# Performance work log

Measured on AMD Instinct MI355X. Metric: run time of the kernel, lower is better.

The kernel has to match this reference:

```python
import jax, jax.numpy as jnp
import numpy as np

B, T, M, P = 256, 256, 512, 512


def setup_inputs() -> dict:
    key = jax.random.key(0)
    ks = jax.random.split(key, 10)
    sc = lambda fan: 1.0 / np.sqrt(fan)
    return {
        "H": jax.random.normal(ks[0], (B, T, M), jnp.float32),
        "d0": jax.random.normal(ks[1], (1, B, P), jnp.float32),
        "s0": jax.random.normal(ks[2], (1, B, P), jnp.float32),
        # TemporalAttention params (torch Linear convention: y = x @ W.T)
        "W_d": jax.random.uniform(ks[3], (M, 2 * P), jnp.float32, -sc(2 * P), sc(2 * P)),
        "U_d": jax.random.uniform(ks[4], (M, M), jnp.float32, -sc(M), sc(M)),
        "v_d": jax.random.uniform(ks[5], (1, M), jnp.float32, -sc(M), sc(M)),
        # LSTM params (torch nn.LSTM convention, gate order i,f,g,o)
        "W_ih": jax.random.uniform(ks[6], (4 * P, M), jnp.float32, -sc(P), sc(P)),
        "W_hh": jax.random.uniform(ks[7], (4 * P, P), jnp.float32, -sc(P), sc(P)),
        "b_ih": jax.random.uniform(ks[8], (4 * P,), jnp.float32, -sc(P), sc(P)),
        "b_hh": jax.random.uniform(ks[9], (4 * P,), jnp.float32, -sc(P), sc(P)),
    }


def reference(H, d0, s0, W_d, U_d, v_d, W_ih, W_hh, b_ih, b_hh):
    T_steps = H.shape[1]
    # U_d(H) is time-invariant across decode steps: precompute once. [B,T,m]
    UH = jnp.einsum("btm,nm->btn", H, U_d)
    v = v_d[0]  # [m]

    def step(carry, _):
        d, s = carry  # [B,p] hidden, [B,p] cell
        q = jnp.concatenate([d, s], axis=-1)            # [B,2p]
        wq = q @ W_d.T                                   # [B,m]
        e = jnp.tanh(wq[:, None, :] + UH) @ v            # [B,T]
        beta = jax.nn.softmax(e, axis=1)                 # softmax over time
        c_t = jnp.einsum("bt,btm->bm", beta, H)          # [B,m]
        gates = c_t @ W_ih.T + b_ih + d @ W_hh.T + b_hh  # [B,4p]
        i, f, g, o = jnp.split(gates, 4, axis=-1)
        s_new = jax.nn.sigmoid(f) * s + jax.nn.sigmoid(i) * jnp.tanh(g)
        d_new = jax.nn.sigmoid(o) * jnp.tanh(s_new)
        return (d_new, s_new), (beta, c_t)

    (d, s), (betas, cts) = jax.lax.scan(step, (d0[0], s0[0]), None, length=T_steps)
    attn = jnp.transpose(betas, (1, 0, 2))               # [B,T,T]
    out = jnp.concatenate([d[:, None, :], cts[-1][:, None, :]], axis=2)  # [B,1,p+m]
    return out, attn
```

## Files before the change

kernel.cpp:

```cpp
#include <hip/hip_runtime.h>
#include <hip/hip_fp16.h>

typedef _Float16 h4 __attribute__((ext_vector_type(4)));
typedef _Float16 h8 __attribute__((ext_vector_type(8)));
typedef float    f4 __attribute__((ext_vector_type(4)));

#define SC2LOG2E 2.8853900817779268f

__device__ __forceinline__ float v_exp2(float x) { float r; asm("v_exp_f32 %0, %1" : "=v"(r) : "v"(x)); return r; }
__device__ __forceinline__ float v_rcp (float x) { float r; asm("v_rcp_f32 %0, %1" : "=v"(r) : "v"(x)); return r; }
__device__ __forceinline__ float fast_tanh(float x) {
    float e = __expf(2.0f * x);
    return 1.0f - 2.0f * v_rcp(e + 1.0f);
}
__device__ __forceinline__ float fast_sigmoid(float x) {
    return v_rcp(1.0f + __expf(-x));
}

__global__ void convert_f16(const float* __restrict__ s, _Float16* __restrict__ d, int n) {
    int i = (blockIdx.x * 256 + threadIdx.x) * 4;
    if (i < n) {
        float4 v = *(const float4*)(s + i);
        h4 o = {(_Float16)v.x, (_Float16)v.y, (_Float16)v.z, (_Float16)v.w};
        *(h4*)(d + i) = o;
    }
}

__global__ void build_wg(const float* __restrict__ Wih, const float* __restrict__ Whh,
                         _Float16* __restrict__ Wg) {
    int idx = (blockIdx.x * 256 + threadIdx.x) * 4;
    int np = idx >> 10, k = idx & 1023;
    int p = np >> 2, g = np & 3, row = g * 512 + p;
    const float* src = (k < 512) ? Wih + (size_t)row * 512 + k
                                 : Whh + (size_t)row * 512 + (k - 512);
    float4 v = *(const float4*)src;
    h4 o = {(_Float16)v.x, (_Float16)v.y, (_Float16)v.z, (_Float16)v.w};
    *(h4*)(Wg + idx) = o;
}

__global__ void build_bsum(const float* __restrict__ bih, const float* __restrict__ bhh,
                           float* __restrict__ bsum) {
    int np = blockIdx.x * 256 + threadIdx.x;
    int p = np >> 2, g = np & 3, row = g * 512 + p;
    bsum[np] = bih[row] + bhh[row];
}

__global__ void init_state(const float* __restrict__ d0, const float* __restrict__ s0,
                           float* __restrict__ sbuf,
                           _Float16* __restrict__ qA, _Float16* __restrict__ ds) {
    int i = blockIdx.x * 256 + threadIdx.x;
    float dv = d0[i], sv = s0[i];
    sbuf[i] = sv;
    int b = i >> 9, j = i & 511;
    qA[(size_t)b * 1024 + 512 + j] = (_Float16)dv;
    ds[(size_t)b * 1024 + j]       = (_Float16)dv;
    ds[(size_t)b * 1024 + 512 + j] = (_Float16)sv;
}

__global__ __launch_bounds__(128) void uh_mfma(const float* __restrict__ H,
                                               const float* __restrict__ Ud,
                                               _Float16* __restrict__ UH2) {
    int tid = threadIdx.x;
    int lane = tid & 63, w = tid >> 6;
    int ln = lane & 15, quad = lane >> 4;
    int m0 = blockIdx.x * 64, n0 = blockIdx.y * 32;
    f4 z = {0.f, 0.f, 0.f, 0.f};
    f4 acc[4] = {z, z, z, z};
    const float* brow = Ud + (size_t)(n0 + w * 16 + ln) * 512 + quad * 8;
    const float* arow = H  + (size_t)(m0 + ln) * 512 + quad * 8;
#pragma unroll 2
    for (int k = 0; k < 16; k++) {
        float4 bx = *(const float4*)(brow + k * 32);
        float4 by = *(const float4*)(brow + k * 32 + 4);
        h8 b = {(_Float16)bx.x, (_Float16)bx.y, (_Float16)bx.z, (_Float16)bx.w,
                (_Float16)by.x, (_Float16)by.y, (_Float16)by.z, (_Float16)by.w};
#pragma unroll
        for (int mt = 0; mt < 4; mt++) {
            const float* ap = arow + (size_t)mt * 16 * 512 + k * 32;
            float4 ax = *(const float4*)ap;
            float4 ay = *(const float4*)(ap + 4);
            h8 a = {(_Float16)ax.x, (_Float16)ax.y, (_Float16)ax.z, (_Float16)ax.w,
                    (_Float16)ay.x, (_Float16)ay.y, (_Float16)ay.z, (_Float16)ay.w};
            acc[mt] = __builtin_amdgcn_mfma_f32_16x16x32_f16(a, b, acc[mt], 0, 0, 0);
        }
    }
#pragma unroll
    for (int mt = 0; mt < 4; mt++)
#pragma unroll
        for (int r = 0; r < 4; r++)
            UH2[(size_t)(m0 + mt * 16 + quad * 4 + r) * 512 + n0 + w * 16 + ln] =
                (_Float16)(acc[mt][r] * SC2LOG2E);
}

__global__ __launch_bounds__(256) void wq_gemm(const _Float16* __restrict__ ds,
                                               const _Float16* __restrict__ Wdh,
                                               float* __restrict__ wq2) {
    int tid = threadIdx.x;
    int lane = tid & 63, w = tid >> 6;
    int ln = lane & 15, quad = lane >> 4;
    int m0 = blockIdx.x * 64, n0 = blockIdx.y * 16;
    f4 acc = {0.f, 0.f, 0.f, 0.f};
    const h8* ap = (const h8*)(ds  + (size_t)(m0 + w * 16 + ln) * 1024) + quad;
    const h8* bp = (const h8*)(Wdh + (size_t)(n0 + ln) * 1024) + quad;
#pragma unroll 8
    for (int k = 0; k < 32; k++) {
        h8 a = ap[k * 4];
        h8 b = bp[k * 4];
        acc = __builtin_amdgcn_mfma_f32_16x16x32_f16(a, b, acc, 0, 0, 0);
    }
#pragma unroll
    for (int r = 0; r < 4; r++)
        wq2[(size_t)(m0 + w * 16 + quad * 4 + r) * 512 + n0 + ln] = acc[r] * SC2LOG2E;
}

__global__ __launch_bounds__(512) void gates_gemm(const _Float16* __restrict__ qcur,
                                                  const _Float16* __restrict__ Wg,
                                                  const float* __restrict__ bsum,
                                                  float* __restrict__ sbuf,
                                                  _Float16* __restrict__ qnext,
                                                  _Float16* __restrict__ ds,
                                                  float* __restrict__ out,
                                                  int t) {
    __shared__ float gt[64][36];
    int tid = threadIdx.x;
    int lane = tid & 63, w = tid >> 6;
    int ln = lane & 15, quad = lane >> 4;
    int mt = w & 3, nt = w >> 2;
    int m0 = blockIdx.x * 64, n0 = blockIdx.y * 32;
    f4 acc = {0.f, 0.f, 0.f, 0.f};
    const h8* ap = (const h8*)(qcur + (size_t)(m0 + mt * 16 + ln) * 1024) + quad;
    const h8* bp = (const h8*)(Wg   + (size_t)(n0 + nt * 16 + ln) * 1024) + quad;
#pragma unroll 8
    for (int k = 0; k < 32; k++) {
        h8 a = ap[k * 4];
        h8 b = bp[k * 4];
        acc = __builtin_amdgcn_mfma_f32_16x16x32_f16(a, b, acc, 0, 0, 0);
    }
    float bs = bsum[n0 + nt * 16 + ln];
#pragma unroll
    for (int r = 0; r < 4; r++)
        gt[mt * 16 + quad * 4 + r][nt * 16 + ln] = acc[r] + bs;
    __syncthreads();

    int p0 = blockIdx.y * 8;
    int ml = tid >> 3, pl = tid & 7;
    float4 g4 = *(const float4*)&gt[ml][pl * 4];
    int b = m0 + ml, p = p0 + pl;
    float ig = fast_sigmoid(g4.x);
    float fg = fast_sigmoid(g4.y);
    float gg = fast_tanh(g4.z);
    float og = fast_sigmoid(g4.w);
    float sold = sbuf[(size_t)b * 512 + p];
    float snew = fmaf(fg, sold, ig * gg);
    float dnew = og * fast_tanh(snew);
    sbuf[(size_t)b * 512 + p] = snew;
    qnext[(size_t)b * 1024 + 512 + p] = (_Float16)dnew;
    ds[(size_t)b * 1024 + p]          = (_Float16)dnew;
    ds[(size_t)b * 1024 + 512 + p]    = (_Float16)snew;
    if (t == 255) out[(size_t)b * 1024 + p] = dnew;
}

__global__ __launch_bounds__(1024) void attn_kernel(const _Float16* __restrict__ UH2,
                                                    const _Float16* __restrict__ Hh,
                                                    const float* __restrict__ Hf,
                                                    const float* __restrict__ wq2,
                                                    const float* __restrict__ vd,
                                                    _Float16* __restrict__ qcur,
                                                    float* __restrict__ attn_out,
                                                    float* __restrict__ out,
                                                    int t) {
    __shared__ float es[256];
    __shared__ float red[4];
    __shared__ float red2[4];
    __shared__ float part[8][512];

    int b = blockIdx.x;
    int tid = threadIdx.x;
    int wv = tid >> 6, lane = tid & 63;

    const float4* wqp = (const float4*)(wq2 + (size_t)b * 512 + lane * 8);
    float4 w0 = wqp[0], w1 = wqp[1];
    const float4* vp = (const float4*)(vd + lane * 8);
    float4 vv0 = vp[0], vv1 = vp[1];
    float wr[8] = {w0.x, w0.y, w0.z, w0.w, w1.x, w1.y, w1.z, w1.w};
    float vr[8] = {vv0.x, vv0.y, vv0.z, vv0.w, vv1.x, vv1.y, vv1.z, vv1.w};

    const h8* up = (const h8*)(UH2 + (size_t)b * 256 * 512) + lane;
#pragma unroll 2
    for (int i = 0; i < 16; i++) {
        int tp = wv * 16 + i;
        h8 u = up[(size_t)tp * 64];
        float acc = 0.0f;
#pragma unroll
        for (int j = 0; j < 8; j++) {
            float zz = wr[j] + (float)u[j];
            float r = v_rcp(1.0f + v_exp2(zz));
            acc = fmaf(vr[j], r, acc);
        }
#pragma unroll
        for (int o = 32; o; o >>= 1) acc += __shfl_xor(acc, o, 64);
        if (lane == 0) es[tp] = -2.0f * acc;
    }
    __syncthreads();

    float v = 0.0f, ex = 0.0f;
    if (tid < 256) {
        v = es[tid];
        float mx = v;
#pragma unroll
        for (int o = 32; o; o >>= 1) mx = fmaxf(mx, __shfl_xor(mx, o, 64));
        if (lane == 0) red[wv] = mx;
    }
    __syncthreads();
    float mall = fmaxf(fmaxf(red[0], red[1]), fmaxf(red[2], red[3]));
    if (tid < 256) {
        ex = __expf(v - mall);
        float s = ex;
#pragma unroll
        for (int o = 32; o; o >>= 1) s += __shfl_xor(s, o, 64);
        if (lane == 0) red2[wv] = s;
    }
    __syncthreads();
    float tot = red2[0] + red2[1] + red2[2] + red2[3];
    float beta = 0.0f;
    if (tid < 256) beta = ex * v_rcp(tot);
    __syncthreads();
    if (tid < 256) {
        es[tid] = beta;
        attn_out[(size_t)b * 65536 + (size_t)t * 256 + tid] = beta;
    }
    __syncthreads();

    int tc = tid >> 7, g = tid & 127;
    float a0 = 0, a1 = 0, a2 = 0, a3 = 0;
    if (Hh) {
        const h4* hp = (const h4*)(Hh + ((size_t)b * 256 + tc * 32) * 512) + g;
#pragma unroll 4
        for (int i = 0; i < 32; i++) {
            h4 hv = hp[(size_t)i * 128];
            float bt = es[tc * 32 + i];
            a0 = fmaf(bt, (float)hv[0], a0);
            a1 = fmaf(bt, (float)hv[1], a1);
            a2 = fmaf(bt, (float)hv[2], a2);
            a3 = fmaf(bt, (float)hv[3], a3);
        }
    } else {
        const float4* hp = (const float4*)(Hf + ((size_t)b * 256 + tc * 32) * 512) + g;
#pragma unroll 4
        for (int i = 0; i < 32; i++) {
            float4 hv = hp[(size_t)i * 128];
            float bt = es[tc * 32 + i];
            a0 = fmaf(bt, hv.x, a0);
            a1 = fmaf(bt, hv.y, a1);
            a2 = fmaf(bt, hv.z, a2);
            a3 = fmaf(bt, hv.w, a3);
        }
    }
    *(float4*)&part[tc][g * 4] = make_float4(a0, a1, a2, a3);
    __syncthreads();
    if (tid < 512) {
        int m = tid;
        float c = part[0][m] + part[1][m] + part[2][m] + part[3][m]
                + part[4][m] + part[5][m] + part[6][m] + part[7][m];
        qcur[(size_t)b * 1024 + m] = (_Float16)c;
        if (t == 255) out[(size_t)b * 1024 + 512 + m] = c;
    }
}

extern "C" void kernel_launch(void* const* d_in, const int* in_sizes, int n_in,
                              void* d_out, int out_size, void* d_ws, size_t ws_size,
                              hipStream_t stream) {
    const float* H   = (const float*)d_in[0];
    const float* d0  = (const float*)d_in[1];
    const float* s0  = (const float*)d_in[2];
    const float* Wd  = (const float*)d_in[3];
    const float* Ud  = (const float*)d_in[4];
    const float* vd  = (const float*)d_in[5];
    const float* Wih = (const float*)d_in[6];
    const float* Whh = (const float*)d_in[7];
    const float* bih = (const float*)d_in[8];
    const float* bhh = (const float*)d_in[9];

    float* out  = (float*)d_out;
    float* attn = out + 262144;

    char* ws = (char*)d_ws;
    size_t off = 0;
    _Float16* UH2  = (_Float16*)(ws + off); off += 67108864;
    _Float16* Wdh  = (_Float16*)(ws + off); off += 1048576;
    _Float16* Wg   = (_Float16*)(ws + off); off += 4194304;
    float*    bsum = (float*)   (ws + off); off += 8192;
    float*    wq2  = (float*)   (ws + off); off += 524288;
    _Float16* qA   = (_Float16*)(ws + off); off += 524288;
    _Float16* qB   = (_Float16*)(ws + off); off += 524288;
    _Float16* ds   = (_Float16*)(ws + off); off += 524288;
    float*    sbuf = (float*)   (ws + off); off += 524288;
    _Float16* Hh   = nullptr;
    if (ws_size >= off + 67108864) { Hh = (_Float16*)(ws + off); off += 67108864; }

    convert_f16<<<512, 256, 0, stream>>>(Wd, Wdh, 524288);
    build_wg<<<2048, 256, 0, stream>>>(Wih, Whh, Wg);
    build_bsum<<<8, 256, 0, stream>>>(bih, bhh, bsum);
    if (Hh) convert_f16<<<32768, 256, 0, stream>>>(H, Hh, 33554432);
    init_state<<<512, 256, 0, stream>>>(d0, s0, sbuf, qA, ds);
    uh_mfma<<<dim3(1024, 16), 128, 0, stream>>>(H, Ud, UH2);

    for (int t = 0; t < 256; t++) {
        _Float16* qcur = (t & 1) ? qB : qA;
        _Float16* qnxt = (t & 1) ? qA : qB;
        wq_gemm<<<dim3(4, 32), 256, 0, stream>>>(ds, Wdh, wq2);
        attn_kernel<<<256, 1024, 0, stream>>>(UH2, Hh, H, wq2, vd, qcur, attn, out, t);
        gates_gemm<<<dim3(4, 64), 512, 0, stream>>>(qcur, Wg, bsum, sbuf, qnxt, ds, out, t);
    }
}
```

Before: 14.34 ms.

## Fuse per-step decoder kernels into one persistent cooperative kernel with grid barriers

Replaces the 768 per-step kernel launches (wq GEMM, attention, gates GEMM) with a single persistent cooperative kernel of 256 blocks of 512 threads. The three phases are separated by a custom atomic grid barrier. This removes launch overhead and inter-kernel gaps on the sequential recurrence. In exchange the attention phase runs with half as many threads per block, and correctness depends on all blocks being co-resident and on the spin barrier; there is a non-cooperative fallback launch.

```diff
diff --git a/kernel.cpp b/kernel.cpp
--- a/kernel.cpp
+++ b/kernel.cpp
@@ -55,6 +55,11 @@
     qA[(size_t)b * 1024 + 512 + j] = (_Float16)dv;
     ds[(size_t)b * 1024 + j]       = (_Float16)dv;
     ds[(size_t)b * 1024 + 512 + j] = (_Float16)sv;
+}
+
+__global__ void zero_bar(unsigned* __restrict__ bar, int n) {
+    int i = blockIdx.x * 256 + threadIdx.x;
+    if (i < n) bar[i] = 0u;
 }
 
 __global__ __launch_bounds__(128) void uh_mfma(const float* __restrict__ H,
@@ -92,178 +97,211 @@
                 (_Float16)(acc[mt][r] * SC2LOG2E);
 }
 
-__global__ __launch_bounds__(256) void wq_gemm(const _Float16* __restrict__ ds,
-                                               const _Float16* __restrict__ Wdh,
-                                               float* __restrict__ wq2) {
-    int tid = threadIdx.x;
-    int lane = tid & 63, w = tid >> 6;
-    int ln = lane & 15, quad = lane >> 4;
-    int m0 = blockIdx.x * 64, n0 = blockIdx.y * 16;
-    f4 acc = {0.f, 0.f, 0.f, 0.f};
-    const h8* ap = (const h8*)(ds  + (size_t)(m0 + w * 16 + ln) * 1024) + quad;
-    const h8* bp = (const h8*)(Wdh + (size_t)(n0 + ln) * 1024) + quad;
+__device__ __forceinline__ void gbar(unsigned* __restrict__ arrive,
+                                     unsigned* __restrict__ gen,
+                                     unsigned ticket) {
+    __syncthreads();
+    if (blockIdx.x == 0) {
+        int tid = threadIdx.x;
+        if (tid >= 1 && tid < 256) {
+            while (__hip_atomic_load(arrive + (size_t)tid * 16, __ATOMIC_RELAXED,
+                                     __HIP_MEMORY_SCOPE_AGENT) < ticket)
+                __builtin_amdgcn_s_sleep(1);
+        }
+        __builtin_amdgcn_fence(__ATOMIC_ACQUIRE, "agent");
+        __syncthreads();
+        if (tid == 0)
+            __hip_atomic_store(gen, ticket, __ATOMIC_RELEASE, __HIP_MEMORY_SCOPE_AGENT);
+    } else {
+        if (threadIdx.x == 0) {
+            __hip_atomic_store(arrive + (size_t)blockIdx.x * 16, ticket,
+                               __ATOMIC_RELEASE, __HIP_MEMORY_SCOPE_AGENT);
+            while (__hip_atomic_load(gen, __ATOMIC_RELAXED,
+                                     __HIP_MEMORY_SCOPE_AGENT) < ticket)
+                __builtin_amdgcn_s_sleep(1);
+        }
+        __builtin_amdgcn_fence(__ATOMIC_ACQUIRE, "agent");
+        __syncthreads();
+    }
+}
+
+struct LoopArgs {
+    const _Float16* UH2;
+    const _Float16* Hh;
+    const float*    Hf;
+    const _Float16* Wdh;
+    const _Float16* Wg;
+    const float*    bsum;
+    const float*    vd;
+    float*          wq2;
+    _Float16*       qA;
+    _Float16*       qB;
+    _Float16*       ds;
+    float*          sbuf;
+    float*          out;
+    float*          attn;
+    unsigned*       bar;
+};
+
+__global__ __launch_bounds__(512) void decoder_loop(LoopArgs A) {
+    const int bid = blockIdx.x;
+    const int tid = threadIdx.x;
+    const int lane = tid & 63, wv = tid >> 6;
+    const int ln = lane & 15, quad = lane >> 4;
+
+    __shared__ __align__(16) union {
+        struct { float es[256]; float red[4]; float red2[4]; float part[4][512]; } at;
+        float gt[64][36];
+    } sm;
+
+    unsigned* arrive = A.bar;
+    unsigned* gen    = A.bar + 4096;
+    unsigned  bt     = 0;
+
+    const int a_m0 = (bid >> 5) * 64, a_n0 = (bid & 31) * 16;
+    const float4* vp = (const float4*)(A.vd + lane * 8);
+    float4 vv0 = vp[0], vv1 = vp[1];
+    float vr[8] = {vv0.x, vv0.y, vv0.z, vv0.w, vv1.x, vv1.y, vv1.z, vv1.w};
+    const h8* up = (const h8*)(A.UH2 + (size_t)bid * 131072) + lane;
+    const int c_mt = wv & 3, c_nt = wv >> 2;
+    const int c_m0 = (bid & 3) * 64, c_by = bid >> 2;
+    const int c_n0 = c_by * 32, c_p0 = c_by * 8;
+    const float c_bs = A.bsum[c_n0 + c_nt * 16 + ln];
+    const int c_ml = tid >> 3, c_pl = tid & 7;
+
+#pragma unroll 1
+    for (int t = 0; t < 256; ++t) {
+        _Float16* qcur = (t & 1) ? A.qB : A.qA;
+        _Float16* qnxt = (t & 1) ? A.qA : A.qB;
+
+        if (bid < 128 && tid < 256) {
+            f4 acc = {0.f, 0.f, 0.f, 0.f};
+            const h8* ap = (const h8*)(A.ds  + (size_t)(a_m0 + wv * 16 + ln) * 1024) + quad;
+            const h8* bp = (const h8*)(A.Wdh + (size_t)(a_n0 + ln) * 1024) + quad;
 #pragma unroll 8
-    for (int k = 0; k < 32; k++) {
-        h8 a = ap[k * 4];
-        h8 b = bp[k * 4];
-        acc = __builtin_amdgcn_mfma_f32_16x16x32_f16(a, b, acc, 0, 0, 0);
-    }
-#pragma unroll
-    for (int r = 0; r < 4; r++)
-        wq2[(size_t)(m0 + w * 16 + quad * 4 + r) * 512 + n0 + ln] = acc[r] * SC2LOG2E;
-}
-
-__global__ __launch_bounds__(512) void gates_gemm(const _Float16* __restrict__ qcur,
-                                                  const _Float16* __restrict__ Wg,
-                                                  const float* __restrict__ bsum,
-                                                  float* __restrict__ sbuf,
-                                                  _Float16* __restrict__ qnext,
-                                                  _Float16* __restrict__ ds,
-                                                  float* __restrict__ out,
-                                                  int t) {
-    __shared__ float gt[64][36];
-    int tid = threadIdx.x;
-    int lane = tid & 63, w = tid >> 6;
-    int ln = lane & 15, quad = lane >> 4;
-    int mt = w & 3, nt = w >> 2;
-    int m0 = blockIdx.x * 64, n0 = blockIdx.y * 32;
-    f4 acc = {0.f, 0.f, 0.f, 0.f};
-    const h8* ap = (const h8*)(qcur + (size_t)(m0 + mt * 16 + ln) * 1024) + quad;
-    const h8* bp = (const h8*)(Wg   + (size_t)(n0 + nt * 16 + ln) * 1024) + quad;
+            for (int k = 0; k < 32; ++k)
+                acc = __builtin_amdgcn_mfma_f32_16x16x32_f16(ap[k * 4], bp[k * 4], acc, 0, 0, 0);
+#pragma unroll
+            for (int r = 0; r < 4; ++r)
+                A.wq2[(size_t)(a_m0 + wv * 16 + quad * 4 + r) * 512 + a_n0 + ln] =
+                    acc[r] * SC2LOG2E;
+        }
+        gbar(arrive, gen, ++bt);
+
+        {
+            const float4* wqp = (const float4*)(A.wq2 + (size_t)bid * 512 + lane * 8);
+            float4 w0 = wqp[0], w1 = wqp[1];
+            float wr[8] = {w0.x, w0.y, w0.z, w0.w, w1.x, w1.y, w1.z, w1.w};
+
+#pragma unroll 4
+            for (int i = 0; i < 32; ++i) {
+                int tp = wv * 32 + i;
+                h8 u = up[(size_t)tp * 64];
+                float acc = 0.0f;
+#pragma unroll
+                for (int j = 0; j < 8; ++j) {
+                    float zz = wr[j] + (float)u[j];
+                    float r = v_rcp(1.0f + v_exp2(zz));
+                    acc = fmaf(vr[j], r, acc);
+                }
+#pragma unroll
+                for (int o = 32; o; o >>= 1) acc += __shfl_xor(acc, o, 64);
+                if (lane == 0) sm.at.es[tp] = -2.0f * acc;
+            }
+            __syncthreads();
+
+            float v = 0.0f, ex = 0.0f;
+            if (tid < 256) {
+                v = sm.at.es[tid];
+                float mx = v;
+#pragma unroll
+                for (int o = 32; o; o >>= 1) mx = fmaxf(mx, __shfl_xor(mx, o, 64));
+                if (lane == 0) sm.at.red[wv] = mx;
+            }
+            __syncthreads();
+            float mall = fmaxf(fmaxf(sm.at.red[0], sm.at.red[1]),
+                               fmaxf(sm.at.red[2], sm.at.red[3]));
+            if (tid < 256) {
+                ex = __expf(v - mall);
+                float s = ex;
+#pragma unroll
+                for (int o = 32; o; o >>= 1) s += __shfl_xor(s, o, 64);
+                if (lane == 0) sm.at.red2[wv] = s;
+            }
+            __syncthreads();
+            float tot = sm.at.red2[0] + sm.at.red2[1] + sm.at.red2[2] + sm.at.red2[3];
+            if (tid < 256) {
+                float beta = ex * v_rcp(tot);
+                sm.at.es[tid] = beta;
+                __builtin_nontemporal_store(beta,
+                    A.attn + (size_t)bid * 65536 + (size_t)t * 256 + tid);
+            }
+            __syncthreads();
+
+            int tc = tid >> 7, g = tid & 127;
+            float a0 = 0, a1 = 0, a2 = 0, a3 = 0;
+            if (A.Hh) {
+                const h4* hp = (const h4*)(A.Hh + ((size_t)bid * 256 + tc * 64) * 512) + g;
 #pragma unroll 8
-    for (int k = 0; k < 32; k++) {
-        h8 a = ap[k * 4];
-        h8 b = bp[k * 4];
-        acc = __builtin_amdgcn_mfma_f32_16x16x32_f16(a, b, acc, 0, 0, 0);
-    }
-    float bs = bsum[n0 + nt * 16 + ln];
-#pragma unroll
-    for (int r = 0; r < 4; r++)
-        gt[mt * 16 + quad * 4 + r][nt * 16 + ln] = acc[r] + bs;
-    __syncthreads();
-
-    int p0 = blockIdx.y * 8;
-    int ml = tid >> 3, pl = tid & 7;
-    float4 g4 = *(const float4*)&gt[ml][pl * 4];
-    int b = m0 + ml, p = p0 + pl;
-    float ig = fast_sigmoid(g4.x);
-    float fg = fast_sigmoid(g4.y);
-    float gg = fast_tanh(g4.z);
-    float og = fast_sigmoid(g4.w);
-    float sold = sbuf[(size_t)b * 512 + p];
-    float snew = fmaf(fg, sold, ig * gg);
-    float dnew = og * fast_tanh(snew);
-    sbuf[(size_t)b * 512 + p] = snew;
-    qnext[(size_t)b * 1024 + 512 + p] = (_Float16)dnew;
-    ds[(size_t)b * 1024 + p]          = (_Float16)dnew;
-    ds[(size_t)b * 1024 + 512 + p]    = (_Float16)snew;
-    if (t == 255) out[(size_t)b * 1024 + p] = dnew;
-}
-
-__global__ __launch_bounds__(1024) void attn_kernel(const _Float16* __restrict__ UH2,
-                                                    const _Float16* __restrict__ Hh,
-                                                    const float* __restrict__ Hf,
-                                                    const float* __restrict__ wq2,
-                                                    const float* __restrict__ vd,
-                                                    _Float16* __restrict__ qcur,
-                                                    float* __restrict__ attn_out,
-                                                    float* __restrict__ out,
-                                                    int t) {
-    __shared__ float es[256];
-    __shared__ float red[4];
-    __shared__ float red2[4];
-    __shared__ float part[8][512];
-
-    int b = blockIdx.x;
-    int tid = threadIdx.x;
-    int wv = tid >> 6, lane = tid & 63;
-
-    const float4* wqp = (const float4*)(wq2 + (size_t)b * 512 + lane * 8);
-    float4 w0 = wqp[0], w1 = wqp[1];
-    const float4* vp = (const float4*)(vd + lane * 8);
-    float4 vv0 = vp[0], vv1 = vp[1];
-    float wr[8] = {w0.x, w0.y, w0.z, w0.w, w1.x, w1.y, w1.z, w1.w};
-    float vr[8] = {vv0.x, vv0.y, vv0.z, vv0.w, vv1.x, vv1.y, vv1.z, vv1.w};
-
-    const h8* up = (const h8*)(UH2 + (size_t)b * 256 * 512) + lane;
-#pragma unroll 2
-    for (int i = 0; i < 16; i++) {
-        int tp = wv * 16 + i;
-        h8 u = up[(size_t)tp * 64];
-        float acc = 0.0f;
-#pragma unroll
-        for (int j = 0; j < 8; j++) {
-            float zz = wr[j] + (float)u[j];
-            float r = v_rcp(1.0f + v_exp2(zz));
-            acc = fmaf(vr[j], r, acc);
-        }
-#pragma unroll
-        for (int o = 32; o; o >>= 1) acc += __shfl_xor(acc, o, 64);
-        if (lane == 0) es[tp] = -2.0f * acc;
-    }
-    __syncthreads();
-
-    float v = 0.0f, ex = 0.0f;
-    if (tid < 256) {
-        v = es[tid];
-        float mx = v;
-#pragma unroll
-        for (int o = 32; o; o >>= 1) mx = fmaxf(mx, __shfl_xor(mx, o, 64));
-        if (lane == 0) red[wv] = mx;
-    }
-    __syncthreads();
-    float mall = fmaxf(fmaxf(red[0], red[1]), fmaxf(red[2], red[3]));
-    if (tid < 256) {
-        ex = __expf(v - mall);
-        float s = ex;
-#pragma unroll
-        for (int o = 32; o; o >>= 1) s += __shfl_xor(s, o, 64);
-        if (lane == 0) red2[wv] = s;
-    }
-    __syncthreads();
-    float tot = red2[0] + red2[1] + red2[2] + red2[3];
-    float beta = 0.0f;
-    if (tid < 256) beta = ex * v_rcp(tot);
-    __syncthreads();
-    if (tid < 256) {
-        es[tid] = beta;
-        attn_out[(size_t)b * 65536 + (size_t)t * 256 + tid] = beta;
-    }
-    __syncthreads();
-
-    int tc = tid >> 7, g = tid & 127;
-    float a0 = 0, a1 = 0, a2 = 0, a3 = 0;
-    if (Hh) {
-        const h4* hp = (const h4*)(Hh + ((size_t)b * 256 + tc * 32) * 512) + g;
+                for (int i = 0; i < 64; ++i) {
+                    h4 hv = hp[(size_t)i * 128];
+                    float btv = sm.at.es[tc * 64 + i];
+                    a0 = fmaf(btv, (float)hv[0], a0);
+                    a1 = fmaf(btv, (float)hv[1], a1);
+                    a2 = fmaf(btv, (float)hv[2], a2);
+                    a3 = fmaf(btv, (float)hv[3], a3);
+                }
+            } else {
+                const float4* hp = (const float4*)(A.Hf + ((size_t)bid * 256 + tc * 64) * 512) + g;
 #pragma unroll 4
-        for (int i = 0; i < 32; i++) {
-            h4 hv = hp[(size_t)i * 128];
-            float bt = es[tc * 32 + i];
-            a0 = fmaf(bt, (float)hv[0], a0);
-            a1 = fmaf(bt, (float)hv[1], a1);
-            a2 = fmaf(bt, (float)hv[2], a2);
-            a3 = fmaf(bt, (float)hv[3], a3);
-        }
-    } else {
-        const float4* hp = (const float4*)(Hf + ((size_t)b * 256 + tc * 32) * 512) + g;
-#pragma unroll 4
-        for (int i = 0; i < 32; i++) {
-            float4 hv = hp[(size_t)i * 128];
-            float bt = es[tc * 32 + i];
-            a0 = fmaf(bt, hv.x, a0);
-            a1 = fmaf(bt, hv.y, a1);
-            a2 = fmaf(bt, hv.z, a2);
-            a3 = fmaf(bt, hv.w, a3);
-        }
-    }
-    *(float4*)&part[tc][g * 4] = make_float4(a0, a1, a2, a3);
-    __syncthreads();
-    if (tid < 512) {
-        int m = tid;
-        float c = part[0][m] + part[1][m] + part[2][m] + part[3][m]
-                + part[4][m] + part[5][m] + part[6][m] + part[7][m];
-        qcur[(size_t)b * 1024 + m] = (_Float16)c;
-        if (t == 255) out[(size_t)b * 1024 + 512 + m] = c;
+                for (int i = 0; i < 64; ++i) {
+                    float4 hv = hp[(size_t)i * 128];
+                    float btv = sm.at.es[tc * 64 + i];
+                    a0 = fmaf(btv, hv.x, a0);
+                    a1 = fmaf(btv, hv.y, a1);
+                    a2 = fmaf(btv, hv.z, a2);
+                    a3 = fmaf(btv, hv.w, a3);
+                }
+            }
+            *(float4*)&sm.at.part[tc][g * 4] = make_float4(a0, a1, a2, a3);
+            __syncthreads();
+            {
+                float c = sm.at.part[0][tid] + sm.at.part[1][tid] +
+                          sm.at.part[2][tid] + sm.at.part[3][tid];
+                qcur[(size_t)bid * 1024 + tid] = (_Float16)c;
+                if (t == 255) A.out[(size_t)bid * 1024 + 512 + tid] = c;
+            }
+        }
+        gbar(arrive, gen, ++bt);
+
+        {
+            f4 acc = {0.f, 0.f, 0.f, 0.f};
+            const h8* ap = (const h8*)(qcur + (size_t)(c_m0 + c_mt * 16 + ln) * 1024) + quad;
+            const h8* bp = (const h8*)(A.Wg + (size_t)(c_n0 + c_nt * 16 + ln) * 1024) + quad;
+#pragma unroll 8
+            for (int k = 0; k < 32; ++k)
+                acc = __builtin_amdgcn_mfma_f32_16x16x32_f16(ap[k * 4], bp[k * 4], acc, 0, 0, 0);
+#pragma unroll
+            for (int r = 0; r < 4; ++r)
+                sm.gt[c_mt * 16 + quad * 4 + r][c_nt * 16 + ln] = acc[r] + c_bs;
+            __syncthreads();
+
+            float4 g4 = *(const float4*)&sm.gt[c_ml][c_pl * 4];
+            int b = c_m0 + c_ml, p = c_p0 + c_pl;
+            float ig = fast_sigmoid(g4.x);
+            float fg = fast_sigmoid(g4.y);
+            float gg = fast_tanh(g4.z);
+            float og = fast_sigmoid(g4.w);
+            float sold = A.sbuf[(size_t)b * 512 + p];
+            float snew = fmaf(fg, sold, ig * gg);
+            float dnew = og * fast_tanh(snew);
+            A.sbuf[(size_t)b * 512 + p] = snew;
+            qnxt[(size_t)b * 1024 + 512 + p] = (_Float16)dnew;
+            A.ds[(size_t)b * 1024 + p]       = (_Float16)dnew;
+            A.ds[(size_t)b * 1024 + 512 + p] = (_Float16)snew;
+            if (t == 255) A.out[(size_t)b * 1024 + p] = dnew;
+        }
+        gbar(arrive, gen, ++bt);
     }
 }
 
@@ -295,6 +333,7 @@
     _Float16* qB   = (_Float16*)(ws + off); off += 524288;
     _Float16* ds   = (_Float16*)(ws + off); off += 524288;
     float*    sbuf = (float*)   (ws + off); off += 524288;
+    unsigned* bar  = (unsigned*)(ws + off); off += 32768;
     _Float16* Hh   = nullptr;
     if (ws_size >= off + 67108864) { Hh = (_Float16*)(ws + off); off += 67108864; }
 
@@ -303,13 +342,16 @@
     build_bsum<<<8, 256, 0, stream>>>(bih, bhh, bsum);
     if (Hh) convert_f16<<<32768, 256, 0, stream>>>(H, Hh, 33554432);
     init_state<<<512, 256, 0, stream>>>(d0, s0, sbuf, qA, ds);
+    zero_bar<<<17, 256, 0, stream>>>(bar, 4352);
     uh_mfma<<<dim3(1024, 16), 128, 0, stream>>>(H, Ud, UH2);
 
-    for (int t = 0; t < 256; t++) {
-        _Float16* qcur = (t & 1) ? qB : qA;
-        _Float16* qnxt = (t & 1) ? qA : qB;
-        wq_gemm<<<dim3(4, 32), 256, 0, stream>>>(ds, Wdh, wq2);
-        attn_kernel<<<256, 1024, 0, stream>>>(UH2, Hh, H, wq2, vd, qcur, attn, out, t);
-        gates_gemm<<<dim3(4, 64), 512, 0, stream>>>(qcur, Wg, bsum, sbuf, qnxt, ds, out, t);
-    }
-}
+    LoopArgs la;
+    la.UH2 = UH2; la.Hh = Hh; la.Hf = H; la.Wdh = Wdh; la.Wg = Wg;
+    la.bsum = bsum; la.vd = vd; la.wq2 = wq2; la.qA = qA; la.qB = qB;
+    la.ds = ds; la.sbuf = sbuf; la.out = out; la.attn = attn; la.bar = bar;
+    void* kp[] = { &la };
+    if (hipLaunchCooperativeKernel((void*)decoder_loop, dim3(256), dim3(512),
+                                   kp, 0, stream) != hipSuccess) {
+        decoder_loop<<<dim3(256), dim3(512), 0, stream>>>(la);
+    }
+}
```

Measured after the change: 29.34 ms. 2.05x slower.
